# Performance work log

Hardware: AMD Instinct MI355X
Metric: run time of the kernel (lower is better)

The kernel has to match this reference:

```python
import jax, jax.numpy as jnp
import numpy as np

N = 20000   # nodes
E = 320000  # edges (before self-loops)
D = 128     # input_dim
HID = 128   # hidden_dim
HEADS = 4


def _ln(x, g, b):
    mu = x.mean(-1, keepdims=True)
    var = x.var(-1, keepdims=True)
    return (x - mu) * jax.lax.rsqrt(var + 1e-5) * g + b


def _seg_softmax(a, seg, n):
    # numerically-stable segment softmax over destination nodes
    m = jax.ops.segment_max(a, seg, num_segments=n)
    e = jnp.exp(a - m[seg])
    s = jax.ops.segment_sum(e, seg, num_segments=n)
    return e / (s[seg] + 1e-16)


def _gatv2(x, src, dst, Wl, bl, Wr, br, att, bias, heads, c, concat, n):
    # GATv2Conv: e_ij = att . leaky_relu(xl[j] + xr[i]); softmax over i's neighbors
    xl = (x @ Wl + bl).reshape(n, heads, c)
    xr = (x @ Wr + br).reshape(n, heads, c)
    e = jax.nn.leaky_relu(xl[src] + xr[dst], 0.2)        # [E, H, C]
    a = _seg_softmax(jnp.einsum('ehc,hc->eh', e, att), dst, n)
    out = jax.ops.segment_sum(xl[src] * a[:, :, None], dst, num_segments=n)
    out = out.reshape(n, heads * c) if concat else out.mean(1)
    return out + bias


def setup_inputs() -> dict:
    key = jax.random.key(0)
    ks = iter(jax.random.split(key, 64))
    def nrm(shape, s=0.05):
        return jax.random.normal(next(ks), shape, jnp.float32) * s
    d = {}
    d['x'] = jax.random.normal(next(ks), (N, D), jnp.float32)
    d['edge_index'] = jax.random.randint(next(ks), (2, E), 0, N)
    d['fn_g'] = jnp.ones(D); d['fn_b'] = jnp.zeros(D)
    d['W_in'] = nrm((D, HID)); d['b_in'] = jnp.zeros(HID)
    d['Wl1'] = nrm((HID, HEADS * HID)); d['bl1'] = jnp.zeros(HEADS * HID)
    d['Wr1'] = nrm((HID, HEADS * HID)); d['br1'] = jnp.zeros(HEADS * HID)
    d['att1'] = nrm((HEADS, HID)); d['bg1'] = jnp.zeros(HEADS * HID)
    d['Wl2'] = nrm((HEADS * HID, HID)); d['bl2'] = jnp.zeros(HID)
    d['Wr2'] = nrm((HEADS * HID, HID)); d['br2'] = jnp.zeros(HID)
    d['att2'] = nrm((1, HID)); d['bg2'] = jnp.zeros(HID)
    d['ln1_g'] = jnp.ones(HEADS * HID); d['ln1_b'] = jnp.zeros(HEADS * HID)
    d['ln2_g'] = jnp.ones(HID); d['ln2_b'] = jnp.zeros(HID)
    for p in ['rf', 'cf', 'kf']:
        d['W' + p] = nrm((HID, HID)); d['b' + p] = jnp.zeros(HID)
        d[p + '_g'] = jnp.ones(HID); d[p + '_b'] = jnp.zeros(HID)
    d['Wr1h'] = nrm((HID, HID // 2)); d['br1h'] = jnp.zeros(HID // 2)
    d['Wr2h'] = nrm((HID // 2, HID // 4)); d['br2h'] = jnp.zeros(HID // 4)
    d['Wr3h'] = nrm((HID // 4, 1)); d['br3h'] = jnp.zeros(1)
    d['Wc1h'] = nrm((HID, HID // 2)); d['bc1h'] = jnp.zeros(HID // 2)
    d['Wc2h'] = nrm((HID // 2, 2)); d['bc2h'] = jnp.zeros(2)
    d['Wk1h'] = nrm((HID, HID // 2)); d['bk1h'] = jnp.zeros(HID // 2)
    d['Wk2h'] = nrm((HID // 2, 1)); d['bk2h'] = jnp.zeros(1)
    return d


def reference(x, edge_index, fn_g, fn_b, W_in, b_in,
              Wl1, bl1, Wr1, br1, att1, bg1,
              Wl2, bl2, Wr2, br2, att2, bg2,
              ln1_g, ln1_b, ln2_g, ln2_b,
              Wrf, brf, rf_g, rf_b, Wcf, bcf, cf_g, cf_b, Wkf, bkf, kf_g, kf_b,
              Wr1h, br1h, Wr2h, br2h, Wr3h, br3h,
              Wc1h, bc1h, Wc2h, bc2h, Wk1h, bk1h, Wk2h, bk2h):
    n = x.shape[0]
    h = _ln(x, fn_g, fn_b)
    h = jax.nn.relu(h @ W_in + b_in)
    loops = jnp.arange(n)
    src = jnp.concatenate([edge_index[0], loops])
    dst = jnp.concatenate([edge_index[1], loops])
    h = _gatv2(h, src, dst, Wl1, bl1, Wr1, br1, att1, bg1, HEADS, HID, True, n)
    h = jax.nn.elu(_ln(h, ln1_g, ln1_b))
    h = _gatv2(h, src, dst, Wl2, bl2, Wr2, br2, att2, bg2, 1, HID, False, n)
    emb = jax.nn.elu(_ln(h, ln2_g, ln2_b))
    def feat(W, b, g, bb):
        return jax.nn.relu(_ln(emb @ W + b, g, bb))
    rf = feat(Wrf, brf, rf_g, rf_b)
    cf = feat(Wcf, bcf, cf_g, cf_b)
    kf = feat(Wkf, bkf, kf_g, kf_b)
    returns_pred = jnp.tanh(jax.nn.relu(jax.nn.relu(rf @ Wr1h + br1h) @ Wr2h + br2h) @ Wr3h + br3h) * 0.1
    movement_pred = jax.nn.relu(cf @ Wc1h + bc1h) @ Wc2h + bc2h
    ranking_scores = jax.nn.sigmoid(jax.nn.relu(kf @ Wk1h + bk1h) @ Wk2h + bk2h)
    return (returns_pred, movement_pred, ranking_scores, emb)
```

## Files before the change

### kernel.cpp

```cpp
#include <hip/hip_runtime.h>
#include <cmath>

#define DEV __device__ __forceinline__
#define LOG2E 1.44269504088896340736f

typedef __attribute__((ext_vector_type(8))) short short8v;
typedef __attribute__((ext_vector_type(4))) float f32x4;

DEV float lrelu(float v) { return fmaxf(v, 0.2f * v); }
DEV float elu(float v) { return v > 0.f ? v : expm1f(v); }
DEV float plo(unsigned u) { return __uint_as_float(u << 16); }
DEV float phi(unsigned u) { return __uint_as_float(u & 0xffff0000u); }
DEV unsigned short f2bf(float f) {
  unsigned u = __float_as_uint(f);
  unsigned r = (u + 0x7fffu + ((u >> 16) & 1u)) >> 16;
  return (unsigned short)r;
}
DEV unsigned packbf(float a, float b) {
  return (unsigned)f2bf(a) | ((unsigned)f2bf(b) << 16);
}
DEV void unpack8(uint4 u, float* f) {
  f[0] = plo(u.x); f[1] = phi(u.x); f[2] = plo(u.y); f[3] = phi(u.y);
  f[4] = plo(u.z); f[5] = phi(u.z); f[6] = plo(u.w); f[7] = phi(u.w);
}

__global__ void k_count(const int* __restrict__ ei, int* __restrict__ counts,
                        int E0, int ET) {
  int e = blockIdx.x * 256 + threadIdx.x;
  if (e >= ET) return;
  int dst = (e < E0) ? ei[E0 + e] : (e - E0);
  atomicAdd(&counts[dst], 1);
}

__global__ __launch_bounds__(1024) void k_scan2(const int* __restrict__ counts,
                                                int* __restrict__ offs, int n) {
  int t = threadIdx.x;
  int ch = (n + 1023) >> 10;
  int beg = t * ch, end = min(beg + ch, n);
  int loc = 0;
  for (int i = beg; i < end; ++i) loc += counts[i];
  int lane = t & 63, w = t >> 6;
  int v = loc;
#pragma unroll
  for (int m = 1; m < 64; m <<= 1) {
    int u = __shfl_up(v, m);
    if (lane >= m) v += u;
  }
  __shared__ int wsum[16], wpre[16];
  if (lane == 63) wsum[w] = v;
  __syncthreads();
  if (t < 16) {
    int p = 0;
    for (int i = 0; i < t; ++i) p += wsum[i];
    wpre[t] = p;
  }
  __syncthreads();
  int run = wpre[w] + v - loc;
  for (int i = beg; i < end; ++i) { offs[i] = run; run += counts[i]; }
  if (beg < n && end == n) offs[n] = run;
}

__global__ void k_scatter(const int* __restrict__ ei, const int* __restrict__ offs,
                          int* __restrict__ cursor, int* __restrict__ src_s,
                          int E0, int ET) {
  int e = blockIdx.x * 256 + threadIdx.x;
  if (e >= ET) return;
  int src, dst;
  if (e < E0) { src = ei[e]; dst = ei[E0 + e]; }
  else        { src = e - E0; dst = e - E0; }
  int pos = offs[dst] + atomicAdd(&cursor[dst], 1);
  src_s[pos] = src;
}

DEV void pack_one(const float* __restrict__ W, unsigned short* __restrict__ Wp,
                  int K, int N, int idx) {
  if (idx >= K * N) return;
  int j = idx & 7, l = (idx >> 3) & 63, r = idx >> 9;
  int KB = K / 32;
  int tile = r / KB, kb = r - tile * KB;
  int k = kb * 32 + (l >> 4) * 8 + j;
  int col = tile * 16 + (l & 15);
  Wp[idx] = f2bf(W[(size_t)k * N + col]);
}

__global__ void k_pack_all(const float* w0, const float* w1, const float* w2,
                           const float* w3, const float* w4, const float* w5,
                           const float* w6, const float* w7,
                           unsigned short* p0, unsigned short* p1, unsigned short* p2,
                           unsigned short* p3, unsigned short* p4, unsigned short* p5,
                           unsigned short* p6, unsigned short* p7,
                           const float* bl2, const float* br2, float* bcat) {
  int idx = blockIdx.x * 256 + threadIdx.x;
  pack_one(w0, p0, 128, 128, idx);
  pack_one(w1, p1, 128, 512, idx);
  pack_one(w2, p2, 128, 512, idx);
  pack_one(w3, p3, 512, 128, idx);
  pack_one(w4, p4, 512, 128, idx);
  pack_one(w5, p5, 128, 128, idx);
  pack_one(w6, p6, 128, 128, idx);
  pack_one(w7, p7, 128, 128, idx);
  if (idx < 128) bcat[idx] = bl2[idx];
  else if (idx < 256) bcat[idx] = br2[idx - 128];
}

template<int K, int N, int RT, int ACT, bool OF32, bool OB16>
__global__ __launch_bounds__(256) void k_mfma(const unsigned short* __restrict__ A,
                                              const unsigned short* __restrict__ Wp,
                                              const float* __restrict__ bias,
                                              float* __restrict__ Cf,
                                              unsigned short* __restrict__ Cb) {
  constexpr int KB = K / 32;
  constexpr int TPW = N / 64;
  __shared__ short As[RT * KB * 64 * 8];
  int row0 = blockIdx.x * (16 * RT);
  int t = threadIdx.x, lane = t & 63, w = t >> 6;
  for (int idx = t; idx < RT * KB * 64; idx += 256) {
    int r = idx / (KB * 64), rem = idx - r * (KB * 64);
    int kb = rem >> 6, l = rem & 63;
    const short8v* sp = reinterpret_cast<const short8v*>(
        A + (size_t)(row0 + r * 16 + (l & 15)) * K + kb * 32 + (l >> 4) * 8);
    reinterpret_cast<short8v*>(As)[idx] = *sp;
  }
  __syncthreads();
  f32x4 acc[RT][TPW];
#pragma unroll
  for (int r = 0; r < RT; ++r)
#pragma unroll
    for (int j = 0; j < TPW; ++j) acc[r][j] = f32x4{0.f, 0.f, 0.f, 0.f};
  const short8v* Bp = reinterpret_cast<const short8v*>(Wp);
  for (int kb = 0; kb < KB; ++kb) {
    short8v a[RT];
#pragma unroll
    for (int r = 0; r < RT; ++r)
      a[r] = reinterpret_cast<const short8v*>(As)[(r * KB + kb) * 64 + lane];
#pragma unroll
    for (int j = 0; j < TPW; ++j) {
      int tile = w * TPW + j;
      short8v b = Bp[(tile * KB + kb) * 64 + lane];
#pragma unroll
      for (int r = 0; r < RT; ++r)
        acc[r][j] = __builtin_amdgcn_mfma_f32_16x16x32_bf16(a[r], b, acc[r][j], 0, 0, 0);
    }
  }
#pragma unroll
  for (int j = 0; j < TPW; ++j) {
    int col = (w * TPW + j) * 16 + (lane & 15);
    float bs = bias[col];
#pragma unroll
    for (int rt = 0; rt < RT; ++rt)
#pragma unroll
      for (int r = 0; r < 4; ++r) {
        int row = row0 + rt * 16 + (lane >> 4) * 4 + r;
        float v = acc[rt][j][r] + bs;
        if (ACT == 1) v = fmaxf(v, 0.f);
        if (OF32) Cf[(size_t)row * N + col] = v;
        if (OB16) Cb[(size_t)row * N + col] = f2bf(v);
      }
  }
}

template<int C, int ACT, bool OUT16>
__global__ void k_ln(const float* in, void* out, const float* g, const float* b) {
  constexpr int T = (C < 256) ? C : 256;
  constexpr int EPT = C / T;
  int row = blockIdx.x, t = threadIdx.x;
  const float* ip = in + (size_t)row * C;
  float v[EPT];
  float s = 0.f, s2 = 0.f;
#pragma unroll
  for (int e = 0; e < EPT; ++e) { float xv = ip[t + e * T]; v[e] = xv; s += xv; s2 += xv * xv; }
#pragma unroll
  for (int m = 1; m <= 32; m <<= 1) { s += __shfl_xor(s, m); s2 += __shfl_xor(s2, m); }
  __shared__ float w1s[2], w2s[2];
  if (T > 64) {
    if ((t & 63) == 0) { w1s[t >> 6] = s; w2s[t >> 6] = s2; }
    __syncthreads();
    s = w1s[0] + w1s[1];
    s2 = w2s[0] + w2s[1];
  }
  float mu = s * (1.0f / C);
  float var = s2 * (1.0f / C) - mu * mu;
  float rs = rsqrtf(var + 1e-5f);
#pragma unroll
  for (int e = 0; e < EPT; ++e) {
    int c = t + e * T;
    float y = (v[e] - mu) * rs * g[c] + b[c];
    if (ACT == 1) y = fmaxf(y, 0.f);
    if (ACT == 2) y = elu(y);
    if (OUT16) ((unsigned short*)out)[(size_t)row * C + c] = f2bf(y);
    else       ((float*)out)[(size_t)row * C + c] = y;
  }
}

__global__ __launch_bounds__(256) void k_gat1(const int* __restrict__ offs,
                                              const int* __restrict__ src_s,
                                              const uint4* __restrict__ xl4,
                                              const uint4* __restrict__ xr4,
                                              const float* __restrict__ att,
                                              const float* __restrict__ bg,
                                              const float* __restrict__ lg,
                                              const float* __restrict__ lb,
                                              uint4* __restrict__ out4,
                                              int M) {
  int w = threadIdx.x >> 6, lane = threadIdx.x & 63;
  int n = blockIdx.x * 4 + w;
  if (n >= M) return;
  int st = offs[n], en = offs[n + 1];
  int cb = lane * 8;
  uint4 ur = xr4[(size_t)n * 64 + lane];
  float xr[8];
  unpack8(ur, xr);
  float atv[8];
  {
    const float4* atp = reinterpret_cast<const float4*>(att + cb);
    float4 a0 = atp[0], a1 = atp[1];
    atv[0] = a0.x * LOG2E; atv[1] = a0.y * LOG2E; atv[2] = a0.z * LOG2E; atv[3] = a0.w * LOG2E;
    atv[4] = a1.x * LOG2E; atv[5] = a1.y * LOG2E; atv[6] = a1.z * LOG2E; atv[7] = a1.w * LOG2E;
  }
  float m = -3.0e38f, s = 0.f;
  float acc[8];
#pragma unroll
  for (int k = 0; k < 8; ++k) acc[k] = 0.f;
  uint4 u = xl4[(size_t)src_s[st] * 64 + lane];
  for (int i = st; i < en; ++i) {
    uint4 ucur = u;
    int nx = (i + 1 < en) ? i + 1 : i;
    u = xl4[(size_t)src_s[nx] * 64 + lane];
    float xv[8];
    unpack8(ucur, xv);
    float p = 0.f;
#pragma unroll
    for (int k = 0; k < 8; ++k)
      p = fmaf(atv[k], lrelu(xv[k] + xr[k]), p);
    p += __shfl_xor(p, 1);
    p += __shfl_xor(p, 2);
    p += __shfl_xor(p, 4);
    p += __shfl_xor(p, 8);
    if (__all(p <= m)) {
      float we = exp2f(p - m);
      s += we;
#pragma unroll
      for (int k = 0; k < 8; ++k) acc[k] = fmaf(we, xv[k], acc[k]);
    } else {
      float mn = fmaxf(m, p);
      float al = exp2f(m - mn);
      float we = exp2f(p - mn);
      s = fmaf(s, al, we);
#pragma unroll
      for (int k = 0; k < 8; ++k) acc[k] = fmaf(acc[k], al, we * xv[k]);
      m = mn;
    }
  }
  float inv = 1.0f / (s + 1e-16f);
  float v[8];
  float s1 = 0.f, s2 = 0.f;
#pragma unroll
  for (int k = 0; k < 8; ++k) {
    v[k] = fmaf(acc[k], inv, bg[cb + k]);
    s1 += v[k];
    s2 += v[k] * v[k];
  }
#pragma unroll
  for (int mm = 1; mm <= 32; mm <<= 1) { s1 += __shfl_xor(s1, mm); s2 += __shfl_xor(s2, mm); }
  float mu = s1 * (1.0f / 512.0f);
  float var = s2 * (1.0f / 512.0f) - mu * mu;
  float rsd = rsqrtf(var + 1e-5f);
  float y[8];
#pragma unroll
  for (int k = 0; k < 8; ++k)
    y[k] = elu((v[k] - mu) * rsd * lg[cb + k] + lb[cb + k]);
  uint4 o;
  o.x = packbf(y[0], y[1]); o.y = packbf(y[2], y[3]);
  o.z = packbf(y[4], y[5]); o.w = packbf(y[6], y[7]);
  out4[(size_t)n * 64 + lane] = o;
}

__global__ __launch_bounds__(256) void k_gat2(const int* __restrict__ offs,
                                              const int* __restrict__ src_s,
                                              const uint4* __restrict__ xlr4,
                                              const float* __restrict__ att,
                                              const float* __restrict__ bg,
                                              const float* __restrict__ lg,
                                              const float* __restrict__ lb,
                                              float* __restrict__ emb,
                                              uint4* __restrict__ embh4,
                                              int M) {
  int w = threadIdx.x >> 6, lane = threadIdx.x & 63;
  int n = blockIdx.x * 4 + w;
  if (n >= M) return;
  int st = offs[n], en = offs[n + 1];
  int g = lane >> 4, l16 = lane & 15;
  int cb = l16 * 8;
  uint4 ur = xlr4[(size_t)n * 32 + 16 + l16];
  float xr[8];
  unpack8(ur, xr);
  float atv[8];
  {
    const float4* atp = reinterpret_cast<const float4*>(att + cb);
    float4 a0 = atp[0], a1 = atp[1];
    atv[0] = a0.x * LOG2E; atv[1] = a0.y * LOG2E; atv[2] = a0.z * LOG2E; atv[3] = a0.w * LOG2E;
    atv[4] = a1.x * LOG2E; atv[5] = a1.y * LOG2E; atv[6] = a1.z * LOG2E; atv[7] = a1.w * LOG2E;
  }
  float m = -3.0e38f, s = 0.f;
  float acc[8];
#pragma unroll
  for (int k = 0; k < 8; ++k) acc[k] = 0.f;
  int e0 = st + g;
  uint4 u = xlr4[(size_t)src_s[e0 < en ? e0 : en - 1] * 32 + l16];
  for (int i = st; i < en; i += 4) {
    int e = i + g;
    uint4 ucur = u;
    int e2 = i + 4 + g;
    u = xlr4[(size_t)src_s[e2 < en ? e2 : en - 1] * 32 + l16];
    float xv[8];
    unpack8(ucur, xv);
    float p = 0.f;
#pragma unroll
    for (int k = 0; k < 8; ++k)
      p = fmaf(atv[k], lrelu(xv[k] + xr[k]), p);
    p += __shfl_xor(p, 1);
    p += __shfl_xor(p, 2);
    p += __shfl_xor(p, 4);
    p += __shfl_xor(p, 8);
    if (e >= en) p = -3.0e38f;
    if (__all(p <= m)) {
      float we = exp2f(p - m);
      s += we;
#pragma unroll
      for (int k = 0; k < 8; ++k) acc[k] = fmaf(we, xv[k], acc[k]);
    } else {
      float mn = fmaxf(m, p);
      float al = exp2f(m - mn);
      float we = exp2f(p - mn);
      s = fmaf(s, al, we);
#pragma unroll
      for (int k = 0; k < 8; ++k) acc[k] = fmaf(acc[k], al, we * xv[k]);
      m = mn;
    }
  }
#pragma unroll
  for (int d = 16; d < 64; d <<= 1) {
    float mo = __shfl_xor(m, d), so = __shfl_xor(s, d);
    float ao[8];
#pragma unroll
    for (int k = 0; k < 8; ++k) ao[k] = __shfl_xor(acc[k], d);
    float mn = fmaxf(m, mo);
    float e1 = exp2f(m - mn), e2m = exp2f(mo - mn);
    s = s * e1 + so * e2m;
#pragma unroll
    for (int k = 0; k < 8; ++k) acc[k] = acc[k] * e1 + ao[k] * e2m;
    m = mn;
  }
  float inv = 1.0f / (s + 1e-16f);
  float v[8];
  float s1 = 0.f, s2 = 0.f;
#pragma unroll
  for (int k = 0; k < 8; ++k) {
    v[k] = fmaf(acc[k], inv, bg[cb + k]);
    s1 += v[k];
    s2 += v[k] * v[k];
  }
#pragma unroll
  for (int mm = 1; mm <= 32; mm <<= 1) { s1 += __shfl_xor(s1, mm); s2 += __shfl_xor(s2, mm); }
  float mu = s1 * (1.0f / 512.0f);
  float var = s2 * (1.0f / 512.0f) - mu * mu;
  float rsd = rsqrtf(var + 1e-5f);
  if (g == 0) {
    float y[8];
#pragma unroll
    for (int k = 0; k < 8; ++k)
      y[k] = elu((v[k] - mu) * rsd * lg[cb + k] + lb[cb + k]);
    float* ep = emb + (size_t)n * 128 + cb;
    *reinterpret_cast<float4*>(ep)     = float4{y[0], y[1], y[2], y[3]};
    *reinterpret_cast<float4*>(ep + 4) = float4{y[4], y[5], y[6], y[7]};
    uint4 o;
    o.x = packbf(y[0], y[1]); o.y = packbf(y[2], y[3]);
    o.z = packbf(y[4], y[5]); o.w = packbf(y[6], y[7]);
    embh4[(size_t)n * 16 + l16] = o;
  }
}

__global__ __launch_bounds__(256) void k_branch(const unsigned short* __restrict__ A,
    const unsigned short* __restrict__ Wp,
    const float* __restrict__ b0, const float* __restrict__ b1s, const float* __restrict__ b2s,
    const float* __restrict__ g0, const float* __restrict__ gb0,
    const float* __restrict__ g1, const float* __restrict__ gb1,
    const float* __restrict__ g2, const float* __restrict__ gb2,
    float* __restrict__ ff) {
  constexpr int KB = 4, TPW = 6;
  __shared__ short As[KB * 64 * 8];
  __shared__ float Cs[16 * 384];
  int row0 = blockIdx.x * 16;
  int t = threadIdx.x, lane = t & 63, w = t >> 6;
  for (int idx = t; idx < KB * 64; idx += 256) {
    int kb = idx >> 6, l = idx & 63;
    const short8v* sp = reinterpret_cast<const short8v*>(
        A + (size_t)(row0 + (l & 15)) * 128 + kb * 32 + (l >> 4) * 8);
    reinterpret_cast<short8v*>(As)[idx] = *sp;
  }
  __syncthreads();
  f32x4 acc[TPW];
#pragma unroll
  for (int j = 0; j < TPW; ++j) acc[j] = f32x4{0.f, 0.f, 0.f, 0.f};
  const short8v* Bp = reinterpret_cast<const short8v*>(Wp);
  for (int kb = 0; kb < KB; ++kb) {
    short8v a = reinterpret_cast<const short8v*>(As)[kb * 64 + lane];
#pragma unroll
    for (int j = 0; j < TPW; ++j) {
      int tile = w * TPW + j;
      short8v b = Bp[(tile * KB + kb) * 64 + lane];
      acc[j] = __builtin_amdgcn_mfma_f32_16x16x32_bf16(a, b, acc[j], 0, 0, 0);
    }
  }
#pragma unroll
  for (int j = 0; j < TPW; ++j) {
    int col = (w * TPW + j) * 16 + (lane & 15);
    int seg = col >> 7, cl = col & 127;
    const float* bp = (seg == 0) ? b0 : (seg == 1) ? b1s : b2s;
    float bs = bp[cl];
#pragma unroll
    for (int r = 0; r < 4; ++r)
      Cs[((lane >> 4) * 4 + r) * 384 + col] = acc[j][r] + bs;
  }
  __syncthreads();
  int row = t >> 4, l16 = t & 15;
#pragma unroll
  for (int seg = 0; seg < 3; ++seg) {
    float v[8];
    float s = 0.f, s2 = 0.f;
    int base = row * 384 + seg * 128 + l16 * 8;
#pragma unroll
    for (int k = 0; k < 8; ++k) { v[k] = Cs[base + k]; s += v[k]; s2 += v[k] * v[k]; }
#pragma unroll
    for (int mm = 1; mm <= 8; mm <<= 1) { s += __shfl_xor(s, mm); s2 += __shfl_xor(s2, mm); }
    float mu = s * (1.0f / 128.0f);
    float var = s2 * (1.0f / 128.0f) - mu * mu;
    float rsd = rsqrtf(var + 1e-5f);
    const float* gp = (seg == 0) ? g0 : (seg == 1) ? g1 : g2;
    const float* bp = (seg == 0) ? gb0 : (seg == 1) ? gb1 : gb2;
    float* op = ff + (size_t)(row0 + row) * 384 + seg * 128 + l16 * 8;
#pragma unroll
    for (int k = 0; k < 8; ++k) {
      int c = l16 * 8 + k;
      op[k] = fmaxf((v[k] - mu) * rsd * gp[c] + bp[c], 0.f);
    }
  }
}

__global__ __launch_bounds__(256) void k_heads(const float* __restrict__ ff, int nb,
    const float* __restrict__ Wr1h, const float* __restrict__ br1h,
    const float* __restrict__ Wr2h, const float* __restrict__ br2h,
    const float* __restrict__ Wr3h, const float* __restrict__ br3h,
    const float* __restrict__ Wc1h, const float* __restrict__ bc1h,
    const float* __restrict__ Wc2h, const float* __restrict__ bc2h,
    const float* __restrict__ Wk1h, const float* __restrict__ bk1h,
    const float* __restrict__ Wk2h, const float* __restrict__ bk2h,
    float* __restrict__ out_ret, float* __restrict__ out_mov,
    float* __restrict__ out_rank) {
  int type = blockIdx.x / nb;
  int b = blockIdx.x - type * nb;
  __shared__ float sh[4][224];
  int wid = threadIdx.x >> 6, lane = threadIdx.x & 63;
  int row = b * 4 + wid;
  const float* in = ff + (type == 0 ? 0 : (type == 1 ? 128 : 256));
  const float2* rp = reinterpret_cast<const float2*>(in + (size_t)row * 384);
  float2 f2 = rp[lane];
  sh[wid][2 * lane] = f2.x;
  sh[wid][2 * lane + 1] = f2.y;
  __syncthreads();
  const float* W1 = (type == 0) ? Wr1h : (type == 1) ? Wc1h : Wk1h;
  const float* b1 = (type == 0) ? br1h : (type == 1) ? bc1h : bk1h;
  float a = b1[lane];
#pragma unroll 8
  for (int k = 0; k < 128; ++k) a = fmaf(sh[wid][k], W1[k * 64 + lane], a);
  sh[wid][128 + lane] = fmaxf(a, 0.f);
  __syncthreads();
  if (type == 0) {
    if (lane < 32) {
      float a2 = br2h[lane];
#pragma unroll 8
      for (int k = 0; k < 64; ++k) a2 = fmaf(sh[wid][128 + k], Wr2h[k * 32 + lane], a2);
      sh[wid][192 + lane] = fmaxf(a2, 0.f);
    }
    __syncthreads();
    if (lane == 0) {
      float a3 = br3h[0];
#pragma unroll
      for (int k = 0; k < 32; ++k) a3 = fmaf(sh[wid][192 + k], Wr3h[k], a3);
      out_ret[row] = tanhf(a3) * 0.1f;
    }
  } else if (type == 1) {
    if (lane < 2) {
      float a2 = bc2h[lane];
#pragma unroll 8
      for (int k = 0; k < 64; ++k) a2 = fmaf(sh[wid][128 + k], Wc2h[k * 2 + lane], a2);
      out_mov[(size_t)row * 2 + lane] = a2;
    }
  } else {
    if (lane == 0) {
      float a2 = bk2h[0];
#pragma unroll 8
      for (int k = 0; k < 64; ++k) a2 = fmaf(sh[wid][128 + k], Wk2h[k], a2);
      out_rank[row] = 1.0f / (1.0f + expf(-a2));
    }
  }
}

extern "C" void kernel_launch(void* const* d_in, const int* in_sizes, int n_in,
                              void* d_out, int out_size, void* d_ws, size_t ws_size,
                              hipStream_t stream) {
  const float* x     = (const float*)d_in[0];
  const int*   ei    = (const int*)  d_in[1];
  const float* fn_g  = (const float*)d_in[2];
  const float* fn_b  = (const float*)d_in[3];
  const float* W_in  = (const float*)d_in[4];
  const float* b_in  = (const float*)d_in[5];
  const float* Wl1   = (const float*)d_in[6];
  const float* bl1   = (const float*)d_in[7];
  const float* Wr1   = (const float*)d_in[8];
  const float* br1   = (const float*)d_in[9];
  const float* att1  = (const float*)d_in[10];
  const float* bg1   = (const float*)d_in[11];
  const float* Wl2   = (const float*)d_in[12];
  const float* bl2   = (const float*)d_in[13];
  const float* Wr2   = (const float*)d_in[14];
  const float* br2   = (const float*)d_in[15];
  const float* att2  = (const float*)d_in[16];
  const float* bg2   = (const float*)d_in[17];
  const float* ln1_g = (const float*)d_in[18];
  const float* ln1_b = (const float*)d_in[19];
  const float* ln2_g = (const float*)d_in[20];
  const float* ln2_b = (const float*)d_in[21];
  const float* Wrf   = (const float*)d_in[22];
  const float* brf   = (const float*)d_in[23];
  const float* rf_g  = (const float*)d_in[24];
  const float* rf_b  = (const float*)d_in[25];
  const float* Wcf   = (const float*)d_in[26];
  const float* bcf   = (const float*)d_in[27];
  const float* cf_g  = (const float*)d_in[28];
  const float* cf_b  = (const float*)d_in[29];
  const float* Wkf   = (const float*)d_in[30];
  const float* bkf   = (const float*)d_in[31];
  const float* kf_g  = (const float*)d_in[32];
  const float* kf_b  = (const float*)d_in[33];
  const float* Wr1h  = (const float*)d_in[34];
  const float* br1h  = (const float*)d_in[35];
  const float* Wr2h  = (const float*)d_in[36];
  const float* br2h  = (const float*)d_in[37];
  const float* Wr3h  = (const float*)d_in[38];
  const float* br3h  = (const float*)d_in[39];
  const float* Wc1h  = (const float*)d_in[40];
  const float* bc1h  = (const float*)d_in[41];
  const float* Wc2h  = (const float*)d_in[42];
  const float* bc2h  = (const float*)d_in[43];
  const float* Wk1h  = (const float*)d_in[44];
  const float* bk1h  = (const float*)d_in[45];
  const float* Wk2h  = (const float*)d_in[46];
  const float* bk2h  = (const float*)d_in[47];

  const int M  = in_sizes[0] / 128;
  const int E0 = in_sizes[1] / 2;
  const int ET = E0 + M;

  char* base = (char*)d_ws;
  size_t off = 0;
  auto carve = [&](size_t bytes) -> char* {
    off = (off + 255) & ~(size_t)255;
    char* p = base + off;
    off += bytes;
    return p;
  };
  const size_t B512 = (size_t)M * 512 * 2;
  const size_t B256 = (size_t)M * 256 * 2;
  const size_t B128 = (size_t)M * 128 * 2;
  unsigned short* hnh   = (unsigned short*)carve(B128);
  unsigned short* h0h   = (unsigned short*)carve(B128);
  unsigned short* xl1h  = (unsigned short*)carve(B512);
  unsigned short* xr1h  = (unsigned short*)carve(B512);
  unsigned short* g1h   = (unsigned short*)carve(B512);
  unsigned short* xlr2h = (unsigned short*)carve(B256);
  unsigned short* embh  = (unsigned short*)carve(B128);
  int* src_s = (int*)carve((size_t)(ET + 8) * sizeof(int));
  int* cnt   = (int*)carve((size_t)2 * M * sizeof(int));
  int* cur   = cnt + M;
  int* offs  = (int*)carve((size_t)(M + 1) * sizeof(int));
  unsigned short* Winp = (unsigned short*)carve(128 * 128 * 2);
  unsigned short* Wl1p = (unsigned short*)carve(128 * 512 * 2);
  unsigned short* Wr1p = (unsigned short*)carve(128 * 512 * 2);
  unsigned short* Wl2p = (unsigned short*)carve(512 * 128 * 2);
  unsigned short* Wr2p = (unsigned short*)carve(512 * 128 * 2);
  unsigned short* Wtp  = (unsigned short*)carve(3 * 128 * 128 * 2);
  float* bcat = (float*)carve(256 * sizeof(float));
  float* ff = (float*)xl1h;
  (void)ws_size; (void)n_in; (void)out_size; (void)Wr2p;

  hipMemsetAsync(cnt, 0, (size_t)2 * M * sizeof(int), stream);
  k_count<<<(ET + 255) / 256, 256, 0, stream>>>(ei, cnt, E0, ET);
  k_scan2<<<1, 1024, 0, stream>>>(cnt, offs, M);
  k_scatter<<<(ET + 255) / 256, 256, 0, stream>>>(ei, offs, cur, src_s, E0, ET);

  k_pack_all<<<256, 256, 0, stream>>>(W_in, Wl1, Wr1, Wl2, Wr2, Wrf, Wcf, Wkf,
                                      Winp, Wl1p, Wr1p, Wl2p, Wr2p,
                                      Wtp, Wtp + 16384, Wtp + 32768,
                                      bl2, br2, bcat);

  k_ln<128, 0, true><<<M, 128, 0, stream>>>(x, hnh, fn_g, fn_b);
  k_mfma<128, 128, 2, 1, false, true><<<M / 32, 256, 0, stream>>>(hnh, Winp, b_in, nullptr, h0h);
  k_mfma<128, 512, 2, 0, false, true><<<M / 32, 256, 0, stream>>>(h0h, Wl1p, bl1, nullptr, xl1h);
  k_mfma<128, 512, 2, 0, false, true><<<M / 32, 256, 0, stream>>>(h0h, Wr1p, br1, nullptr, xr1h);
  k_gat1<<<(M + 3) / 4, 256, 0, stream>>>(offs, src_s, (const uint4*)xl1h, (const uint4*)xr1h,
                                          att1, bg1, ln1_g, ln1_b, (uint4*)g1h, M);
  k_mfma<512, 256, 2, 0, false, true><<<M / 32, 256, 0, stream>>>(g1h, Wl2p, bcat, nullptr, xlr2h);

  float* out_ret  = (float*)d_out;
  float* out_mov  = out_ret + M;
  float* out_rank = out_ret + 3 * M;
  float* emb      = out_ret + 4 * M;
  k_gat2<<<(M + 3) / 4, 256, 0, stream>>>(offs, src_s, (const uint4*)xlr2h,
                                          att2, bg2, ln2_g, ln2_b, emb, (uint4*)embh, M);

  k_branch<<<M / 16, 256, 0, stream>>>(embh, Wtp, brf, bcf, bkf,
                                       rf_g, rf_b, cf_g, cf_b, kf_g, kf_b, ff);

  int nb = M / 4;
  k_heads<<<3 * nb, 256, 0, stream>>>(ff, nb,
                                      Wr1h, br1h, Wr2h, br2h, Wr3h, br3h,
                                      Wc1h, bc1h, Wc2h, bc2h,
                                      Wk1h, bk1h, Wk2h, bk2h,
                                      out_ret, out_mov, out_rank);
}
```

Baseline: 337.4 us.

## Replace scalar FMA head kernel with block-diagonal bf16 MFMA GEMMs

The three per-branch MLP heads, previously computed with scalar FMAs in a one-row-per-wave kernel, are packed into block-diagonal weight matrices (384x192 and 192x64) and run through the existing MFMA GEMM kernel. A small tail kernel then applies the final 32-wide dot, tanh and sigmoid. The branch features are now stored as bf16, which halves their memory traffic but lowers the precision of the head inputs. The block-diagonal layout spends extra MFMA work on zero blocks in exchange for tensor-core throughput and fewer launches per row.

```diff
diff --git a/kernel.cpp b/kernel.cpp
--- a/kernel.cpp
+++ b/kernel.cpp
@@ -101,6 +101,47 @@
   pack_one(w7, p7, 128, 128, idx);
   if (idx < 128) bcat[idx] = bl2[idx];
   else if (idx < 256) bcat[idx] = br2[idx - 128];
+}
+
+DEV float bd1_val(const float* Wr, const float* Wc, const float* Wk, int k, int col) {
+  int blk = col >> 6;
+  if ((k >> 7) != blk) return 0.f;
+  const float* W = (blk == 0) ? Wr : (blk == 1) ? Wc : Wk;
+  return W[(k & 127) * 64 + (col & 63)];
+}
+DEV float bd2_val(const float* Wr2, const float* Wc2, const float* Wk2, int k, int col) {
+  if (col < 32) return (k < 64) ? Wr2[k * 32 + col] : 0.f;
+  if (col < 34) return (k >= 64 && k < 128) ? Wc2[(k - 64) * 2 + (col - 32)] : 0.f;
+  if (col == 34) return (k >= 128) ? Wk2[k - 128] : 0.f;
+  return 0.f;
+}
+
+__global__ void k_pack_heads(const float* Wr1, const float* Wc1, const float* Wk1,
+                             const float* Wr2, const float* Wc2, const float* Wk2,
+                             const float* br1, const float* bc1, const float* bk1,
+                             const float* br2, const float* bc2, const float* bk2,
+                             unsigned short* P1, unsigned short* P2,
+                             float* bh1, float* bh2) {
+  int idx = blockIdx.x * 256 + threadIdx.x;
+  if (idx < 384 * 192) {
+    int j = idx & 7, l = (idx >> 3) & 63, r = idx >> 9;
+    const int KB = 12;
+    int tile = r / KB, kb = r - tile * KB;
+    int k = kb * 32 + (l >> 4) * 8 + j;
+    int col = tile * 16 + (l & 15);
+    P1[idx] = f2bf(bd1_val(Wr1, Wc1, Wk1, k, col));
+  }
+  if (idx < 192 * 64) {
+    int j = idx & 7, l = (idx >> 3) & 63, r = idx >> 9;
+    const int KB = 6;
+    int tile = r / KB, kb = r - tile * KB;
+    int k = kb * 32 + (l >> 4) * 8 + j;
+    int col = tile * 16 + (l & 15);
+    P2[idx] = f2bf(bd2_val(Wr2, Wc2, Wk2, k, col));
+  }
+  if (idx < 192) bh1[idx] = (idx < 64) ? br1[idx] : (idx < 128) ? bc1[idx - 64] : bk1[idx - 128];
+  if (idx < 64)
+    bh2[idx] = (idx < 32) ? br2[idx] : (idx < 34) ? bc2[idx - 32] : (idx == 34) ? bk2[0] : 0.f;
 }
 
 template<int K, int N, int RT, int ACT, bool OF32, bool OB16>
@@ -386,7 +427,7 @@
     const float* __restrict__ g0, const float* __restrict__ gb0,
     const float* __restrict__ g1, const float* __restrict__ gb1,
     const float* __restrict__ g2, const float* __restrict__ gb2,
-    float* __restrict__ ff) {
+    unsigned* __restrict__ ffh) {
   constexpr int KB = 4, TPW = 6;
   __shared__ short As[KB * 64 * 8];
   __shared__ float Cs[16 * 384];
@@ -438,72 +479,36 @@
     float rsd = rsqrtf(var + 1e-5f);
     const float* gp = (seg == 0) ? g0 : (seg == 1) ? g1 : g2;
     const float* bp = (seg == 0) ? gb0 : (seg == 1) ? gb1 : gb2;
-    float* op = ff + (size_t)(row0 + row) * 384 + seg * 128 + l16 * 8;
+    unsigned* op = ffh + (size_t)(row0 + row) * 192 + seg * 64 + l16 * 4;
+    float y[8];
 #pragma unroll
     for (int k = 0; k < 8; ++k) {
       int c = l16 * 8 + k;
-      op[k] = fmaxf((v[k] - mu) * rsd * gp[c] + bp[c], 0.f);
+      y[k] = fmaxf((v[k] - mu) * rsd * gp[c] + bp[c], 0.f);
     }
-  }
-}
-
-__global__ __launch_bounds__(256) void k_heads(const float* __restrict__ ff, int nb,
-    const float* __restrict__ Wr1h, const float* __restrict__ br1h,
-    const float* __restrict__ Wr2h, const float* __restrict__ br2h,
-    const float* __restrict__ Wr3h, const float* __restrict__ br3h,
-    const float* __restrict__ Wc1h, const float* __restrict__ bc1h,
-    const float* __restrict__ Wc2h, const float* __restrict__ bc2h,
-    const float* __restrict__ Wk1h, const float* __restrict__ bk1h,
-    const float* __restrict__ Wk2h, const float* __restrict__ bk2h,
-    float* __restrict__ out_ret, float* __restrict__ out_mov,
-    float* __restrict__ out_rank) {
-  int type = blockIdx.x / nb;
-  int b = blockIdx.x - type * nb;
-  __shared__ float sh[4][224];
-  int wid = threadIdx.x >> 6, lane = threadIdx.x & 63;
-  int row = b * 4 + wid;
-  const float* in = ff + (type == 0 ? 0 : (type == 1 ? 128 : 256));
-  const float2* rp = reinterpret_cast<const float2*>(in + (size_t)row * 384);
-  float2 f2 = rp[lane];
-  sh[wid][2 * lane] = f2.x;
-  sh[wid][2 * lane + 1] = f2.y;
-  __syncthreads();
-  const float* W1 = (type == 0) ? Wr1h : (type == 1) ? Wc1h : Wk1h;
-  const float* b1 = (type == 0) ? br1h : (type == 1) ? bc1h : bk1h;
-  float a = b1[lane];
-#pragma unroll 8
-  for (int k = 0; k < 128; ++k) a = fmaf(sh[wid][k], W1[k * 64 + lane], a);
-  sh[wid][128 + lane] = fmaxf(a, 0.f);
-  __syncthreads();
-  if (type == 0) {
-    if (lane < 32) {
-      float a2 = br2h[lane];
-#pragma unroll 8
-      for (int k = 0; k < 64; ++k) a2 = fmaf(sh[wid][128 + k], Wr2h[k * 32 + lane], a2);
-      sh[wid][192 + lane] = fmaxf(a2, 0.f);
-    }
-    __syncthreads();
-    if (lane == 0) {
-      float a3 = br3h[0];
-#pragma unroll
-      for (int k = 0; k < 32; ++k) a3 = fmaf(sh[wid][192 + k], Wr3h[k], a3);
-      out_ret[row] = tanhf(a3) * 0.1f;
-    }
-  } else if (type == 1) {
-    if (lane < 2) {
-      float a2 = bc2h[lane];
-#pragma unroll 8
-      for (int k = 0; k < 64; ++k) a2 = fmaf(sh[wid][128 + k], Wc2h[k * 2 + lane], a2);
-      out_mov[(size_t)row * 2 + lane] = a2;
-    }
-  } else {
-    if (lane == 0) {
-      float a2 = bk2h[0];
-#pragma unroll 8
-      for (int k = 0; k < 64; ++k) a2 = fmaf(sh[wid][128 + k], Wk2h[k], a2);
-      out_rank[row] = 1.0f / (1.0f + expf(-a2));
-    }
-  }
+    op[0] = packbf(y[0], y[1]); op[1] = packbf(y[2], y[3]);
+    op[2] = packbf(y[4], y[5]); op[3] = packbf(y[6], y[7]);
+  }
+}
+
+__global__ void k_tail(const float* __restrict__ tmp,
+                       const float* __restrict__ Wr3, const float* __restrict__ br3,
+                       float* __restrict__ out_ret, float* __restrict__ out_mov,
+                       float* __restrict__ out_rank, int M) {
+  int row = blockIdx.x * 256 + threadIdx.x;
+  if (row >= M) return;
+  const float4* tp = reinterpret_cast<const float4*>(tmp + (size_t)row * 64);
+  float4 v[9];
+#pragma unroll
+  for (int q = 0; q < 9; ++q) v[q] = tp[q];
+  const float* tv = reinterpret_cast<const float*>(v);
+  float a3 = br3[0];
+#pragma unroll
+  for (int k = 0; k < 32; ++k) a3 = fmaf(fmaxf(tv[k], 0.f), Wr3[k], a3);
+  out_ret[row] = tanhf(a3) * 0.1f;
+  out_mov[2 * row]     = tv[32];
+  out_mov[2 * row + 1] = tv[33];
+  out_rank[row] = 1.0f / (1.0f + expf(-tv[34]));
 }
 
 extern "C" void kernel_launch(void* const* d_in, const int* in_sizes, int n_in,
@@ -590,8 +595,14 @@
   unsigned short* Wl2p = (unsigned short*)carve(512 * 128 * 2);
   unsigned short* Wr2p = (unsigned short*)carve(512 * 128 * 2);
   unsigned short* Wtp  = (unsigned short*)carve(3 * 128 * 128 * 2);
+  unsigned short* Wh1p = (unsigned short*)carve(384 * 192 * 2);
+  unsigned short* Wh2p = (unsigned short*)carve(192 * 64 * 2);
   float* bcat = (float*)carve(256 * sizeof(float));
-  float* ff = (float*)xl1h;
+  float* bh1  = (float*)carve(192 * sizeof(float));
+  float* bh2  = (float*)carve(64 * sizeof(float));
+  unsigned* ffh = (unsigned*)xl1h;
+  unsigned short* h1h = xr1h;
+  float* tmp = (float*)g1h;
   (void)ws_size; (void)n_in; (void)out_size; (void)Wr2p;
 
   hipMemsetAsync(cnt, 0, (size_t)2 * M * sizeof(int), stream);
@@ -603,6 +614,9 @@
                                       Winp, Wl1p, Wr1p, Wl2p, Wr2p,
                                       Wtp, Wtp + 16384, Wtp + 32768,
                                       bl2, br2, bcat);
+  k_pack_heads<<<288, 256, 0, stream>>>(Wr1h, Wc1h, Wk1h, Wr2h, Wc2h, Wk2h,
+                                        br1h, bc1h, bk1h, br2h, bc2h, bk2h,
+                                        Wh1p, Wh2p, bh1, bh2);
 
   k_ln<128, 0, true><<<M, 128, 0, stream>>>(x, hnh, fn_g, fn_b);
   k_mfma<128, 128, 2, 1, false, true><<<M / 32, 256, 0, stream>>>(hnh, Winp, b_in, nullptr, h0h);
@@ -620,12 +634,12 @@
                                           att2, bg2, ln2_g, ln2_b, emb, (uint4*)embh, M);
 
   k_branch<<<M / 16, 256, 0, stream>>>(embh, Wtp, brf, bcf, bkf,
-                                       rf_g, rf_b, cf_g, cf_b, kf_g, kf_b, ff);
-
-  int nb = M / 4;
-  k_heads<<<3 * nb, 256, 0, stream>>>(ff, nb,
-                                      Wr1h, br1h, Wr2h, br2h, Wr3h, br3h,
-                                      Wc1h, bc1h, Wc2h, bc2h,
-                                      Wk1h, bk1h, Wk2h, bk2h,
-                                      out_ret, out_mov, out_rank);
-}
+                                       rf_g, rf_b, cf_g, cf_b, kf_g, kf_b, ffh);
+
+  k_mfma<384, 192, 2, 1, false, true><<<M / 32, 256, 0, stream>>>(
+      (const unsigned short*)ffh, Wh1p, bh1, nullptr, h1h);
+  k_mfma<192, 64, 2, 0, true, false><<<M / 32, 256, 0, stream>>>(
+      h1h, Wh2p, bh2, tmp, nullptr);
+  k_tail<<<(M + 255) / 256, 256, 0, stream>>>(tmp, Wr3h, br3h,
+                                              out_ret, out_mov, out_rank, M);
+}
```

Result: faster. 285.4 us (-15.4%).
